# Performance work log

Measured on AMD Instinct MI355X. Metric: run time of the kernel, lower is better.

## Reference

```python
import jax, jax.numpy as jnp
import numpy as np

N = 50176
E = 802816
G = 64
IN_DIM = 128
HID = 128
GLOB = 16
BN_EPS = 1e-5


def transformer_conv(x, src, dst, Wq, bq, Wk, bk, Wv, bv, Ws, bs):
    # PyG TransformerConv, heads=1, concat=True, root_weight=True, beta=False
    q = x @ Wq + bq          # [N, H]
    k = x @ Wk + bk          # [N, H]
    v = x @ Wv + bv          # [N, H]
    scale = 1.0 / jnp.sqrt(jnp.asarray(HID, x.dtype))
    logits = jnp.sum(q[dst] * k[src], axis=-1) * scale          # [E]
    m = jax.ops.segment_max(logits, dst, num_segments=N)        # [N]
    m = jnp.where(jnp.isfinite(m), m, 0.0)
    e = jnp.exp(logits - m[dst])                                # [E]
    s = jax.ops.segment_sum(e, dst, num_segments=N)             # [N]
    alpha = e / (s[dst] + 1e-16)                                # [E]
    agg = jax.ops.segment_sum(alpha[:, None] * v[src], dst, num_segments=N)
    return agg + x @ Ws + bs


def batch_norm(x, gamma, beta):
    mu = jnp.mean(x, axis=0)
    var = jnp.mean((x - mu) ** 2, axis=0)
    return gamma * (x - mu) / jnp.sqrt(var + BN_EPS) + beta


def setup_inputs() -> dict:
    key = jax.random.key(0)
    ks = jax.random.split(key, 32)
    d = {}
    d['x'] = jax.random.normal(ks[0], (N, IN_DIM), dtype=jnp.float32)
    d['edge_index'] = jax.random.randint(ks[1], (2, E), 0, N, dtype=jnp.int32)
    d['ptr'] = (jnp.arange(G + 1, dtype=jnp.int32) * (N // G))
    d['global_features'] = jax.random.normal(ks[2], (G, GLOB), dtype=jnp.float32)
    dims = [(IN_DIM, HID), (HID, HID)]
    ki = 3
    for l, (di, do) in enumerate(dims):
        for nm in ['Wq', 'Wk', 'Wv', 'Ws']:
            d[f'{nm}{l}'] = jax.random.normal(ks[ki], (di, do), dtype=jnp.float32) * 0.05; ki += 1
        for nm in ['bq', 'bk', 'bv', 'bs']:
            d[f'{nm}{l}'] = jnp.zeros((do,), dtype=jnp.float32)
        d[f'g{l}'] = jnp.ones((do,), dtype=jnp.float32)
        d[f'be{l}'] = jnp.zeros((do,), dtype=jnp.float32)
    d['fcW'] = jax.random.normal(ks[ki], (HID + GLOB, HID), dtype=jnp.float32) * 0.05; ki += 1
    d['fcb'] = jnp.zeros((HID,), dtype=jnp.float32)
    d['fc2W'] = jax.random.normal(ks[ki], (HID, 1), dtype=jnp.float32) * 0.05; ki += 1
    d['fc2b'] = jnp.zeros((1,), dtype=jnp.float32)
    return d


def reference(x, edge_index, ptr, global_features,
              Wq0, Wk0, Wv0, Ws0, bq0, bk0, bv0, bs0, g0, be0,
              Wq1, Wk1, Wv1, Ws1, bq1, bk1, bv1, bs1, g1, be1,
              fcW, fcb, fc2W, fc2b):
    src, dst = edge_index[0], edge_index[1]
    h = transformer_conv(x, src, dst, Wq0, bq0, Wk0, bk0, Wv0, bv0, Ws0, bs0)
    h = jax.nn.relu(batch_norm(h, g0, be0))
    h = transformer_conv(h, src, dst, Wq1, bq1, Wk1, bk1, Wv1, bv1, Ws1, bs1)
    h = jax.nn.relu(batch_norm(h, g1, be1))
    # broadcast per-graph global features to nodes using ptr boundaries
    graph_id = jnp.searchsorted(ptr, jnp.arange(N, dtype=ptr.dtype), side='right') - 1
    rep = global_features[graph_id]                              # [N, GLOB]
    h = jnp.concatenate([h, rep], axis=1)
    h = jax.nn.relu(h @ fcW + fcb)
    out = h @ fc2W + fc2b                                        # [N, 1]
    return out[:, 0]
```

## Files before the change

### kernel.cpp

```cpp
#include <hip/hip_runtime.h>
#include <math.h>

#define N_NODES 50176
#define N_EDGES 802816
#define HIDDEN  128
#define NGRAPH  64
#define BN_EPS  1e-5f
#define ATT_SCALE 0.08838834764831845f

typedef __attribute__((ext_vector_type(8))) short bf16x8;
typedef __attribute__((ext_vector_type(4))) float f32x4;

__device__ __forceinline__ float bflo(unsigned u) { return __uint_as_float(u << 16); }
__device__ __forceinline__ float bfhi(unsigned u) { return __uint_as_float(u & 0xffff0000u); }
__device__ __forceinline__ unsigned short f2bf(float f) {
    unsigned u = __float_as_uint(f);
    unsigned r = (u + 0x7fffu + ((u >> 16) & 1u)) >> 16;
    return (unsigned short)r;
}

__global__ void hist_kernel(const int* __restrict__ dst, int* __restrict__ cnt) {
    int e = blockIdx.x * 256 + threadIdx.x;
    if (e < N_EDGES) atomicAdd(&cnt[dst[e]], 1);
}

__global__ void scan1_kernel(const int* __restrict__ cnt, int* __restrict__ row_ptr,
                             int* __restrict__ bsum) {
    __shared__ int sh[256];
    int t = threadIdx.x, b = blockIdx.x;
    int base = b * 1024 + t * 4;
    int v0 = cnt[base], v1 = cnt[base + 1], v2 = cnt[base + 2], v3 = cnt[base + 3];
    int tot = v0 + v1 + v2 + v3;
    sh[t] = tot; __syncthreads();
    for (int off = 1; off < 256; off <<= 1) {
        int x = (t >= off) ? sh[t - off] : 0;
        __syncthreads();
        sh[t] += x;
        __syncthreads();
    }
    int excl = sh[t] - tot;
    row_ptr[base]     = excl;
    row_ptr[base + 1] = excl + v0;
    row_ptr[base + 2] = excl + v0 + v1;
    row_ptr[base + 3] = excl + v0 + v1 + v2;
    if (t == 255) bsum[b] = sh[255];
}

__global__ void scan2_kernel(const int* __restrict__ bsum, int* __restrict__ boff,
                             int* __restrict__ row_ptr) {
    int acc = 0;
    for (int i = 0; i < 49; i++) { boff[i] = acc; acc += bsum[i]; }
    row_ptr[N_NODES] = acc;
}

__global__ void scan3_kernel(int* __restrict__ row_ptr, int* __restrict__ cur,
                             const int* __restrict__ boff) {
    int t = threadIdx.x, b = blockIdx.x;
    int base = b * 1024 + t * 4;
    int off = boff[b];
    #pragma unroll
    for (int j = 0; j < 4; j++) {
        int v = row_ptr[base + j] + off;
        row_ptr[base + j] = v;
        cur[base + j] = v;
    }
}

__global__ void scatter_kernel(const int* __restrict__ src, const int* __restrict__ dst,
                               int* __restrict__ cur, int* __restrict__ edge_src) {
    int e = blockIdx.x * 256 + threadIdx.x;
    if (e < N_EDGES) {
        int d = dst[e];
        int slot = atomicAdd(&cur[d], 1);
        edge_src[slot] = src[e];
    }
}

__global__ void wprep_kernel(const float* __restrict__ Wq, const float* __restrict__ Wk,
                             const float* __restrict__ Wv, const float* __restrict__ Ws,
                             unsigned short* __restrict__ WT) {
    int mb = blockIdx.x;
    const float* W = (mb == 0) ? Wq : (mb == 1) ? Wk : (mb == 2) ? Wv : Ws;
    int t = threadIdx.x;
    int k = t >> 1, ch = t & 1;
    #pragma unroll 8
    for (int cc = 0; cc < 64; cc++) {
        int c = ch * 64 + cc;
        WT[((size_t)mb * 128 + c) * 128 + k] = f2bf(W[k * 128 + c]);
    }
}

__global__ __launch_bounds__(256) void gemm_mfma(
    const float* __restrict__ in,
    const unsigned short* __restrict__ WT,
    const float* __restrict__ bq, const float* __restrict__ bk,
    const float* __restrict__ bv, const float* __restrict__ bs,
    float* __restrict__ qb, unsigned short* __restrict__ kvb,
    float* __restrict__ hb,
    const float* __restrict__ bnA, const float* __restrict__ bnB)
{
    __shared__ unsigned char lds[65536];
    int t = threadIdx.x;
    int n0 = blockIdx.x * 128;
    int m  = blockIdx.y;

    {
        int r = t >> 1, seg = t & 1;
        const float* srcp = in + (size_t)(n0 + r) * 128 + seg * 64;
        unsigned rowbase = r * 256;
        unsigned sw = (r & 7) << 4;
        #pragma unroll
        for (int c = 0; c < 8; c++) {
            float4 f0 = *reinterpret_cast<const float4*>(srcp + c * 8);
            float4 f1 = *reinterpret_cast<const float4*>(srcp + c * 8 + 4);
            if (bnA) {
                int kb = seg * 64 + c * 8;
                float4 a0 = *reinterpret_cast<const float4*>(&bnA[kb]);
                float4 a1 = *reinterpret_cast<const float4*>(&bnA[kb + 4]);
                float4 b0 = *reinterpret_cast<const float4*>(&bnB[kb]);
                float4 b1 = *reinterpret_cast<const float4*>(&bnB[kb + 4]);
                f0.x = fmaxf(f0.x * a0.x + b0.x, 0.f);
                f0.y = fmaxf(f0.y * a0.y + b0.y, 0.f);
                f0.z = fmaxf(f0.z * a0.z + b0.z, 0.f);
                f0.w = fmaxf(f0.w * a0.w + b0.w, 0.f);
                f1.x = fmaxf(f1.x * a1.x + b1.x, 0.f);
                f1.y = fmaxf(f1.y * a1.y + b1.y, 0.f);
                f1.z = fmaxf(f1.z * a1.z + b1.z, 0.f);
                f1.w = fmaxf(f1.w * a1.w + b1.w, 0.f);
            }
            uint4 pk;
            pk.x = (unsigned)f2bf(f0.x) | ((unsigned)f2bf(f0.y) << 16);
            pk.y = (unsigned)f2bf(f0.z) | ((unsigned)f2bf(f0.w) << 16);
            pk.z = (unsigned)f2bf(f1.x) | ((unsigned)f2bf(f1.y) << 16);
            pk.w = (unsigned)f2bf(f1.z) | ((unsigned)f2bf(f1.w) << 16);
            unsigned off = (unsigned)(seg * 128 + c * 16);
            *reinterpret_cast<uint4*>(&lds[rowbase + (off ^ sw)]) = pk;
        }
    }
    {
        int r = t >> 1, seg = t & 1;
        const unsigned short* srcp = WT + ((size_t)m * 128 + r) * 128 + seg * 64;
        unsigned rowbase = 32768u + r * 256;
        unsigned sw = (r & 7) << 4;
        #pragma unroll
        for (int c = 0; c < 8; c++) {
            uint4 pk = *reinterpret_cast<const uint4*>(srcp + c * 8);
            unsigned off = (unsigned)(seg * 128 + c * 16);
            *reinterpret_cast<uint4*>(&lds[rowbase + (off ^ sw)]) = pk;
        }
    }
    __syncthreads();

    int lane = t & 63, w = t >> 6;
    int wr = w >> 1, wc = w & 1;
    int lrow = lane & 15, lk = lane >> 4;
    unsigned sw = (unsigned)((lrow & 7) << 4);

    f32x4 acc[4][4] = {};
    #pragma unroll
    for (int ks = 0; ks < 4; ks++) {
        unsigned o = (unsigned)(ks * 64 + lk * 16);
        bf16x8 af[4], bfr[4];
        #pragma unroll
        for (int i = 0; i < 4; i++) {
            unsigned row = wr * 64 + i * 16 + lrow;
            af[i] = *reinterpret_cast<const bf16x8*>(&lds[row * 256 + (o ^ sw)]);
            unsigned col = wc * 64 + i * 16 + lrow;
            bfr[i] = *reinterpret_cast<const bf16x8*>(&lds[32768u + col * 256 + (o ^ sw)]);
        }
        #pragma unroll
        for (int i = 0; i < 4; i++)
            #pragma unroll
            for (int j = 0; j < 4; j++)
                acc[i][j] = __builtin_amdgcn_mfma_f32_16x16x32_bf16(af[i], bfr[j], acc[i][j], 0, 0, 0);
    }

    const float* bias = (m == 0) ? bq : (m == 1) ? bk : (m == 2) ? bv : bs;
    #pragma unroll
    for (int j = 0; j < 4; j++) {
        int c = wc * 64 + j * 16 + lrow;
        float bi = bias[c];
        #pragma unroll
        for (int i = 0; i < 4; i++) {
            #pragma unroll
            for (int r = 0; r < 4; r++) {
                int row = n0 + wr * 64 + i * 16 + lk * 4 + r;
                float v = acc[i][j][r] + bi;
                if (m == 0) {
                    qb[(size_t)row * 128 + c] = v;
                } else if (m == 3) {
                    hb[(size_t)row * 128 + c] = v;
                } else {
                    kvb[(size_t)row * 256 + (m == 1 ? 0 : 128) + c] = f2bf(v);
                }
            }
        }
    }
}

__global__ __launch_bounds__(256) void agg_kernel(
    const float* __restrict__ qb, const unsigned short* __restrict__ kvb,
    const int* __restrict__ row_ptr, const int* __restrict__ edge_src,
    float* __restrict__ hb)
{
    int wave = threadIdx.x >> 6, lane = threadIdx.x & 63;
    int n = blockIdx.x * 4 + wave;
    int quarter = lane >> 4, ql = lane & 15;

    float4 qa = *reinterpret_cast<const float4*>(&qb[(size_t)n * 128 + ql * 8]);
    float4 qc = *reinterpret_cast<const float4*>(&qb[(size_t)n * 128 + ql * 8 + 4]);
    int s0 = row_ptr[n], s1 = row_ptr[n + 1];

    float acc0 = 0.f, acc1 = 0.f, acc2 = 0.f, acc3 = 0.f;
    float acc4 = 0.f, acc5 = 0.f, acc6 = 0.f, acc7 = 0.f;
    float ssum = 0.f;

    for (int j0 = s0; j0 < s1; j0 += 4) {
        int j = j0 + quarter;
        bool act = (j < s1);
        int s = act ? edge_src[j] : 0;
        const uint4* kv4 = reinterpret_cast<const uint4*>(kvb + (size_t)s * 256);
        uint4 kr = kv4[ql];
        uint4 vr = kv4[16 + ql];

        float part = qa.x * bflo(kr.x) + qa.y * bfhi(kr.x)
                   + qa.z * bflo(kr.y) + qa.w * bfhi(kr.y)
                   + qc.x * bflo(kr.z) + qc.y * bfhi(kr.z)
                   + qc.z * bflo(kr.w) + qc.w * bfhi(kr.w);
        part += __shfl_xor(part, 1, 64);
        part += __shfl_xor(part, 2, 64);
        part += __shfl_xor(part, 4, 64);
        part += __shfl_xor(part, 8, 64);

        float wgt = act ? __expf(part * ATT_SCALE) : 0.f;
        ssum += wgt;
        acc0 += wgt * bflo(vr.x); acc1 += wgt * bfhi(vr.x);
        acc2 += wgt * bflo(vr.y); acc3 += wgt * bfhi(vr.y);
        acc4 += wgt * bflo(vr.z); acc5 += wgt * bfhi(vr.z);
        acc6 += wgt * bflo(vr.w); acc7 += wgt * bfhi(vr.w);
    }

    #define XRED(x) { x += __shfl_xor(x, 16, 64); x += __shfl_xor(x, 32, 64); }
    XRED(acc0) XRED(acc1) XRED(acc2) XRED(acc3)
    XRED(acc4) XRED(acc5) XRED(acc6) XRED(acc7)
    XRED(ssum)
    #undef XRED

    if (quarter == 0) {
        float inv = 1.0f / (ssum + 1e-16f);
        float4 h0 = *reinterpret_cast<float4*>(&hb[(size_t)n * 128 + ql * 8]);
        float4 h1 = *reinterpret_cast<float4*>(&hb[(size_t)n * 128 + ql * 8 + 4]);
        h0.x += acc0 * inv; h0.y += acc1 * inv; h0.z += acc2 * inv; h0.w += acc3 * inv;
        h1.x += acc4 * inv; h1.y += acc5 * inv; h1.z += acc6 * inv; h1.w += acc7 * inv;
        *reinterpret_cast<float4*>(&hb[(size_t)n * 128 + ql * 8]) = h0;
        *reinterpret_cast<float4*>(&hb[(size_t)n * 128 + ql * 8 + 4]) = h1;
    }
}

__global__ __launch_bounds__(256) void bn_stats(const float* __restrict__ h,
                                                float* __restrict__ sums,
                                                float* __restrict__ sqs) {
    int t = threadIdx.x;
    int c = t & 127;
    float s = 0.f, q = 0.f;
    int stride = gridDim.x * 256;
    for (int i = blockIdx.x * 256 + t; i < N_NODES * 128; i += stride) {
        float v = h[i];
        s += v; q += v * v;
    }
    __shared__ float sh[256], shq[256];
    sh[t] = s; shq[t] = q;
    __syncthreads();
    if (t < 128) {
        atomicAdd(&sums[c], sh[t] + sh[t + 128]);
        atomicAdd(&sqs[c],  shq[t] + shq[t + 128]);
    }
}

__global__ void bn_final(const float* __restrict__ sums, const float* __restrict__ sqs,
                         const float* __restrict__ g, const float* __restrict__ be,
                         float* __restrict__ a, float* __restrict__ b) {
    int c = threadIdx.x;
    float mean = sums[c] / (float)N_NODES;
    float var  = sqs[c] / (float)N_NODES - mean * mean;
    float inv  = rsqrtf(var + BN_EPS);
    float av   = g[c] * inv;
    a[c] = av;
    b[c] = be[c] - mean * av;
}

__global__ __launch_bounds__(256) void fc_kernel(
    const float* __restrict__ h2, const float* __restrict__ a1, const float* __restrict__ b1,
    const int* __restrict__ ptr, const float* __restrict__ gf,
    const float* __restrict__ fcW, const float* __restrict__ fcb,
    const float* __restrict__ fc2W, const float* __restrict__ fc2b,
    float* __restrict__ out)
{
    __shared__ float hc[8][144];
    __shared__ float red[8][128];
    int t = threadIdx.x;
    int nb = blockIdx.x * 8;

    {
        int node_l = t >> 5, li = t & 31;
        int n = nb + node_l;
        float4 v = *reinterpret_cast<const float4*>(&h2[(size_t)n * 128 + li * 4]);
        float4 av = *reinterpret_cast<const float4*>(&a1[li * 4]);
        float4 bv = *reinterpret_cast<const float4*>(&b1[li * 4]);
        hc[node_l][li * 4 + 0] = fmaxf(v.x * av.x + bv.x, 0.f);
        hc[node_l][li * 4 + 1] = fmaxf(v.y * av.y + bv.y, 0.f);
        hc[node_l][li * 4 + 2] = fmaxf(v.z * av.z + bv.z, 0.f);
        hc[node_l][li * 4 + 3] = fmaxf(v.w * av.w + bv.w, 0.f);
        if (li < 16) {
            int lo = 0, hi = NGRAPH;
            while (lo < hi) {
                int mid = (lo + hi + 1) >> 1;
                if (ptr[mid] <= n) lo = mid; else hi = mid - 1;
            }
            hc[node_l][128 + li] = gf[lo * 16 + li];
        }
    }
    __syncthreads();

    {
        int half = t >> 7, o = t & 127;
        float fb = fcb[o];
        float acc0 = fb, acc1 = fb, acc2 = fb, acc3 = fb;
        const float* h0 = hc[half * 4 + 0];
        const float* h1 = hc[half * 4 + 1];
        const float* h2c = hc[half * 4 + 2];
        const float* h3 = hc[half * 4 + 3];
        #pragma unroll 16
        for (int i = 0; i < 144; i++) {
            float w = fcW[i * 128 + o];
            acc0 += h0[i] * w;
            acc1 += h1[i] * w;
            acc2 += h2c[i] * w;
            acc3 += h3[i] * w;
        }
        float w2 = fc2W[o];
        red[half * 4 + 0][o] = fmaxf(acc0, 0.f) * w2;
        red[half * 4 + 1][o] = fmaxf(acc1, 0.f) * w2;
        red[half * 4 + 2][o] = fmaxf(acc2, 0.f) * w2;
        red[half * 4 + 3][o] = fmaxf(acc3, 0.f) * w2;
    }
    __syncthreads();

    {
        int node_l = t >> 5, li = t & 31;
        float s = red[node_l][li] + red[node_l][li + 32]
                + red[node_l][li + 64] + red[node_l][li + 96];
        s += __shfl_xor(s, 1, 64);
        s += __shfl_xor(s, 2, 64);
        s += __shfl_xor(s, 4, 64);
        s += __shfl_xor(s, 8, 64);
        s += __shfl_xor(s, 16, 64);
        if (li == 0) out[nb + node_l] = s + fc2b[0];
    }
}

extern "C" void kernel_launch(void* const* d_in, const int* in_sizes, int n_in,
                              void* d_out, int out_size, void* d_ws, size_t ws_size,
                              hipStream_t stream)
{
    const float* x   = (const float*)d_in[0];
    const int*   ei  = (const int*)d_in[1];
    const int*   ptr = (const int*)d_in[2];
    const float* gf  = (const float*)d_in[3];
    const float* Wq0 = (const float*)d_in[4];
    const float* Wk0 = (const float*)d_in[5];
    const float* Wv0 = (const float*)d_in[6];
    const float* Ws0 = (const float*)d_in[7];
    const float* bq0 = (const float*)d_in[8];
    const float* bk0 = (const float*)d_in[9];
    const float* bv0 = (const float*)d_in[10];
    const float* bs0 = (const float*)d_in[11];
    const float* g0  = (const float*)d_in[12];
    const float* be0 = (const float*)d_in[13];
    const float* Wq1 = (const float*)d_in[14];
    const float* Wk1 = (const float*)d_in[15];
    const float* Wv1 = (const float*)d_in[16];
    const float* Ws1 = (const float*)d_in[17];
    const float* bq1 = (const float*)d_in[18];
    const float* bk1 = (const float*)d_in[19];
    const float* bv1 = (const float*)d_in[20];
    const float* bs1 = (const float*)d_in[21];
    const float* g1  = (const float*)d_in[22];
    const float* be1 = (const float*)d_in[23];
    const float* fcW = (const float*)d_in[24];
    const float* fcb = (const float*)d_in[25];
    const float* fc2W= (const float*)d_in[26];
    const float* fc2b= (const float*)d_in[27];
    float* out = (float*)d_out;

    const int* src_p = ei;
    const int* dst_p = ei + N_EDGES;

    char* w = (char*)d_ws;
    const size_t NM = (size_t)N_NODES * 128 * sizeof(float);
    float* qb = (float*)w;                    w += NM;
    unsigned short* kvb = (unsigned short*)w; w += (size_t)N_NODES * 256 * sizeof(unsigned short);
    float* h1 = (float*)w;                    w += NM;
    float* h2 = (float*)w;                    w += NM;
    float* stats = (float*)w;                 w += 1024 * sizeof(float);
    float* sums0 = stats;
    float* sqs0  = stats + 128;
    float* sums1 = stats + 256;
    float* sqs1  = stats + 384;
    float* a0    = stats + 512;
    float* b0    = stats + 640;
    float* a1    = stats + 768;
    float* b1    = stats + 896;
    unsigned short* WT0 = (unsigned short*)w; w += (size_t)512 * 128 * sizeof(unsigned short);
    unsigned short* WT1 = (unsigned short*)w; w += (size_t)512 * 128 * sizeof(unsigned short);
    int* cnt     = (int*)w;                   w += (size_t)N_NODES * sizeof(int);
    int* row_ptr = (int*)w;                   w += (size_t)(N_NODES + 1) * sizeof(int);
    int* cur     = (int*)w;                   w += (size_t)N_NODES * sizeof(int);
    int* edge_src= (int*)w;                   w += (size_t)N_EDGES * sizeof(int);
    int* bsum    = (int*)w;                   w += 64 * sizeof(int);
    int* boff    = (int*)w;                   w += 64 * sizeof(int);

    hipMemsetAsync(cnt, 0, (size_t)N_NODES * sizeof(int), stream);
    hipMemsetAsync(stats, 0, 512 * sizeof(float), stream);

    wprep_kernel<<<4, 256, 0, stream>>>(Wq0, Wk0, Wv0, Ws0, WT0);
    wprep_kernel<<<4, 256, 0, stream>>>(Wq1, Wk1, Wv1, Ws1, WT1);

    hist_kernel<<<3136, 256, 0, stream>>>(dst_p, cnt);
    scan1_kernel<<<49, 256, 0, stream>>>(cnt, row_ptr, bsum);
    scan2_kernel<<<1, 1, 0, stream>>>(bsum, boff, row_ptr);
    scan3_kernel<<<49, 256, 0, stream>>>(row_ptr, cur, boff);
    scatter_kernel<<<3136, 256, 0, stream>>>(src_p, dst_p, cur, edge_src);

    gemm_mfma<<<dim3(392, 4), 256, 0, stream>>>(x, WT0,
        bq0, bk0, bv0, bs0, qb, kvb, h1, nullptr, nullptr);
    agg_kernel<<<12544, 256, 0, stream>>>(qb, kvb, row_ptr, edge_src, h1);
    bn_stats<<<784, 256, 0, stream>>>(h1, sums0, sqs0);
    bn_final<<<1, 128, 0, stream>>>(sums0, sqs0, g0, be0, a0, b0);

    gemm_mfma<<<dim3(392, 4), 256, 0, stream>>>(h1, WT1,
        bq1, bk1, bv1, bs1, qb, kvb, h2, a0, b0);
    agg_kernel<<<12544, 256, 0, stream>>>(qb, kvb, row_ptr, edge_src, h2);
    bn_stats<<<784, 256, 0, stream>>>(h2, sums1, sqs1);
    bn_final<<<1, 128, 0, stream>>>(sums1, sqs1, g1, be1, a1, b1);

    fc_kernel<<<6272, 256, 0, stream>>>(h2, a1, b1, ptr, gf,
        fcW, fcb, fc2W, fc2b, out);
}
```

Baseline: 561.3 us.

## Compute all four projections per block from one shared input tile

The GEMM kernel is restructured so each 512-thread block loads a 64-row input tile once (with fused BN+ReLU and bf16 conversion) and its eight waves compute all four Q/K/V/skip projections, instead of launching a separate block per projection that reloads and reconverts the input. Weight fragments are now read directly from global memory (likely cache-resident) rather than staged in LDS. The K/V bf16 outputs are staged through a swizzled LDS buffer so they can be written to global memory as coalesced 16-byte stores. This cuts input reads and BN work fourfold, at the cost of more global weight traffic per wave and an extra barrier.

```diff
diff --git a/kernel.cpp b/kernel.cpp
--- a/kernel.cpp
+++ b/kernel.cpp
@@ -90,7 +90,7 @@
     }
 }
 
-__global__ __launch_bounds__(256) void gemm_mfma(
+__global__ __launch_bounds__(512, 4) void gemm_mfma(
     const float* __restrict__ in,
     const unsigned short* __restrict__ WT,
     const float* __restrict__ bq, const float* __restrict__ bk,
@@ -99,74 +99,71 @@
     float* __restrict__ hb,
     const float* __restrict__ bnA, const float* __restrict__ bnB)
 {
-    __shared__ unsigned char lds[65536];
+    __shared__ unsigned char ldsA[16384];
+    __shared__ unsigned char ldsKV[32768];
     int t = threadIdx.x;
-    int n0 = blockIdx.x * 128;
-    int m  = blockIdx.y;
+    int n0 = blockIdx.x * 64;
 
     {
-        int r = t >> 1, seg = t & 1;
-        const float* srcp = in + (size_t)(n0 + r) * 128 + seg * 64;
-        unsigned rowbase = r * 256;
-        unsigned sw = (r & 7) << 4;
-        #pragma unroll
-        for (int c = 0; c < 8; c++) {
-            float4 f0 = *reinterpret_cast<const float4*>(srcp + c * 8);
-            float4 f1 = *reinterpret_cast<const float4*>(srcp + c * 8 + 4);
-            if (bnA) {
-                int kb = seg * 64 + c * 8;
-                float4 a0 = *reinterpret_cast<const float4*>(&bnA[kb]);
-                float4 a1 = *reinterpret_cast<const float4*>(&bnA[kb + 4]);
-                float4 b0 = *reinterpret_cast<const float4*>(&bnB[kb]);
-                float4 b1 = *reinterpret_cast<const float4*>(&bnB[kb + 4]);
-                f0.x = fmaxf(f0.x * a0.x + b0.x, 0.f);
-                f0.y = fmaxf(f0.y * a0.y + b0.y, 0.f);
-                f0.z = fmaxf(f0.z * a0.z + b0.z, 0.f);
-                f0.w = fmaxf(f0.w * a0.w + b0.w, 0.f);
-                f1.x = fmaxf(f1.x * a1.x + b1.x, 0.f);
-                f1.y = fmaxf(f1.y * a1.y + b1.y, 0.f);
-                f1.z = fmaxf(f1.z * a1.z + b1.z, 0.f);
-                f1.w = fmaxf(f1.w * a1.w + b1.w, 0.f);
-            }
-            uint4 pk;
-            pk.x = (unsigned)f2bf(f0.x) | ((unsigned)f2bf(f0.y) << 16);
-            pk.y = (unsigned)f2bf(f0.z) | ((unsigned)f2bf(f0.w) << 16);
-            pk.z = (unsigned)f2bf(f1.x) | ((unsigned)f2bf(f1.y) << 16);
-            pk.w = (unsigned)f2bf(f1.z) | ((unsigned)f2bf(f1.w) << 16);
-            unsigned off = (unsigned)(seg * 128 + c * 16);
-            *reinterpret_cast<uint4*>(&lds[rowbase + (off ^ sw)]) = pk;
-        }
-    }
-    {
-        int r = t >> 1, seg = t & 1;
-        const unsigned short* srcp = WT + ((size_t)m * 128 + r) * 128 + seg * 64;
-        unsigned rowbase = 32768u + r * 256;
-        unsigned sw = (r & 7) << 4;
-        #pragma unroll
-        for (int c = 0; c < 8; c++) {
-            uint4 pk = *reinterpret_cast<const uint4*>(srcp + c * 8);
-            unsigned off = (unsigned)(seg * 128 + c * 16);
-            *reinterpret_cast<uint4*>(&lds[rowbase + (off ^ sw)]) = pk;
-        }
+        int r = t >> 3, seg = t & 7;
+        const float* srcp = in + (size_t)(n0 + r) * 128 + seg * 16;
+        float4 f0 = *reinterpret_cast<const float4*>(srcp);
+        float4 f1 = *reinterpret_cast<const float4*>(srcp + 4);
+        float4 f2 = *reinterpret_cast<const float4*>(srcp + 8);
+        float4 f3 = *reinterpret_cast<const float4*>(srcp + 12);
+        if (bnA) {
+            int kb = seg * 16;
+            float4 a0 = *reinterpret_cast<const float4*>(&bnA[kb]);
+            float4 a1 = *reinterpret_cast<const float4*>(&bnA[kb + 4]);
+            float4 a2 = *reinterpret_cast<const float4*>(&bnA[kb + 8]);
+            float4 a3 = *reinterpret_cast<const float4*>(&bnA[kb + 12]);
+            float4 b0 = *reinterpret_cast<const float4*>(&bnB[kb]);
+            float4 b1 = *reinterpret_cast<const float4*>(&bnB[kb + 4]);
+            float4 b2 = *reinterpret_cast<const float4*>(&bnB[kb + 8]);
+            float4 b3 = *reinterpret_cast<const float4*>(&bnB[kb + 12]);
+            f0.x = fmaxf(f0.x * a0.x + b0.x, 0.f); f0.y = fmaxf(f0.y * a0.y + b0.y, 0.f);
+            f0.z = fmaxf(f0.z * a0.z + b0.z, 0.f); f0.w = fmaxf(f0.w * a0.w + b0.w, 0.f);
+            f1.x = fmaxf(f1.x * a1.x + b1.x, 0.f); f1.y = fmaxf(f1.y * a1.y + b1.y, 0.f);
+            f1.z = fmaxf(f1.z * a1.z + b1.z, 0.f); f1.w = fmaxf(f1.w * a1.w + b1.w, 0.f);
+            f2.x = fmaxf(f2.x * a2.x + b2.x, 0.f); f2.y = fmaxf(f2.y * a2.y + b2.y, 0.f);
+            f2.z = fmaxf(f2.z * a2.z + b2.z, 0.f); f2.w = fmaxf(f2.w * a2.w + b2.w, 0.f);
+            f3.x = fmaxf(f3.x * a3.x + b3.x, 0.f); f3.y = fmaxf(f3.y * a3.y + b3.y, 0.f);
+            f3.z = fmaxf(f3.z * a3.z + b3.z, 0.f); f3.w = fmaxf(f3.w * a3.w + b3.w, 0.f);
+        }
+        uint4 p0, p1;
+        p0.x = (unsigned)f2bf(f0.x) | ((unsigned)f2bf(f0.y) << 16);
+        p0.y = (unsigned)f2bf(f0.z) | ((unsigned)f2bf(f0.w) << 16);
+        p0.z = (unsigned)f2bf(f1.x) | ((unsigned)f2bf(f1.y) << 16);
+        p0.w = (unsigned)f2bf(f1.z) | ((unsigned)f2bf(f1.w) << 16);
+        p1.x = (unsigned)f2bf(f2.x) | ((unsigned)f2bf(f2.y) << 16);
+        p1.y = (unsigned)f2bf(f2.z) | ((unsigned)f2bf(f2.w) << 16);
+        p1.z = (unsigned)f2bf(f3.x) | ((unsigned)f2bf(f3.y) << 16);
+        p1.w = (unsigned)f2bf(f3.z) | ((unsigned)f2bf(f3.w) << 16);
+        unsigned sw = (unsigned)((r & 7) << 4);
+        *reinterpret_cast<uint4*>(&ldsA[r * 256 + (((unsigned)(seg * 32)) ^ sw)]) = p0;
+        *reinterpret_cast<uint4*>(&ldsA[r * 256 + (((unsigned)(seg * 32 + 16)) ^ sw)]) = p1;
     }
     __syncthreads();
 
     int lane = t & 63, w = t >> 6;
-    int wr = w >> 1, wc = w & 1;
+    int m = w >> 1, half = w & 1;
     int lrow = lane & 15, lk = lane >> 4;
-    unsigned sw = (unsigned)((lrow & 7) << 4);
 
     f32x4 acc[4][4] = {};
     #pragma unroll
     for (int ks = 0; ks < 4; ks++) {
-        unsigned o = (unsigned)(ks * 64 + lk * 16);
-        bf16x8 af[4], bfr[4];
+        bf16x8 bfr[4], af[4];
+        #pragma unroll
+        for (int j = 0; j < 4; j++) {
+            int col = half * 64 + j * 16 + lrow;
+            bfr[j] = *reinterpret_cast<const bf16x8*>(
+                &WT[((size_t)m * 128 + col) * 128 + ks * 32 + lk * 8]);
+        }
         #pragma unroll
         for (int i = 0; i < 4; i++) {
-            unsigned row = wr * 64 + i * 16 + lrow;
-            af[i] = *reinterpret_cast<const bf16x8*>(&lds[row * 256 + (o ^ sw)]);
-            unsigned col = wc * 64 + i * 16 + lrow;
-            bfr[i] = *reinterpret_cast<const bf16x8*>(&lds[32768u + col * 256 + (o ^ sw)]);
+            unsigned row = (unsigned)(i * 16 + lrow);
+            af[i] = *reinterpret_cast<const bf16x8*>(
+                &ldsA[row * 256 + (((unsigned)(ks * 64 + lk * 16)) ^ ((row & 7) << 4))]);
         }
         #pragma unroll
         for (int i = 0; i < 4; i++)
@@ -176,24 +173,48 @@
     }
 
     const float* bias = (m == 0) ? bq : (m == 1) ? bk : (m == 2) ? bv : bs;
-    #pragma unroll
-    for (int j = 0; j < 4; j++) {
-        int c = wc * 64 + j * 16 + lrow;
-        float bi = bias[c];
-        #pragma unroll
-        for (int i = 0; i < 4; i++) {
+    if (m == 0 || m == 3) {
+        float* ob = (m == 0) ? qb : hb;
+        #pragma unroll
+        for (int j = 0; j < 4; j++) {
+            int c = half * 64 + j * 16 + lrow;
+            float bi = bias[c];
             #pragma unroll
-            for (int r = 0; r < 4; r++) {
-                int row = n0 + wr * 64 + i * 16 + lk * 4 + r;
-                float v = acc[i][j][r] + bi;
-                if (m == 0) {
-                    qb[(size_t)row * 128 + c] = v;
-                } else if (m == 3) {
-                    hb[(size_t)row * 128 + c] = v;
-                } else {
-                    kvb[(size_t)row * 256 + (m == 1 ? 0 : 128) + c] = f2bf(v);
+            for (int i = 0; i < 4; i++)
+                #pragma unroll
+                for (int r4 = 0; r4 < 4; r4++) {
+                    int row = n0 + i * 16 + lk * 4 + r4;
+                    ob[(size_t)row * 128 + c] = acc[i][j][r4] + bi;
                 }
-            }
+        }
+    } else {
+        unsigned vOff = (m == 1) ? 0u : 256u;
+        #pragma unroll
+        for (int j = 0; j < 4; j++) {
+            int c = half * 64 + j * 16 + lrow;
+            float bi = bias[c];
+            unsigned bir = vOff + (unsigned)c * 2;
+            #pragma unroll
+            for (int i = 0; i < 4; i++)
+                #pragma unroll
+                for (int r4 = 0; r4 < 4; r4++) {
+                    unsigned row = (unsigned)(i * 16 + lk * 4 + r4);
+                    unsigned sw = ((row >> 2) & 3) << 5;
+                    *reinterpret_cast<unsigned short*>(&ldsKV[row * 512 + (bir ^ sw)]) =
+                        f2bf(acc[i][j][r4] + bi);
+                }
+        }
+    }
+    __syncthreads();
+    {
+        int r = t >> 3, seg = t & 7;
+        unsigned sw = (((unsigned)r >> 2) & 3) << 5;
+        char* dst = (char*)(kvb + (size_t)(n0 + r) * 256) + seg * 64;
+        #pragma unroll
+        for (int u = 0; u < 4; u++) {
+            uint4 v = *reinterpret_cast<const uint4*>(
+                &ldsKV[r * 512 + (((unsigned)(seg * 64 + u * 16)) ^ sw)]);
+            *reinterpret_cast<uint4*>(dst + u * 16) = v;
         }
     }
 }
@@ -432,13 +453,13 @@
     scan3_kernel<<<49, 256, 0, stream>>>(row_ptr, cur, boff);
     scatter_kernel<<<3136, 256, 0, stream>>>(src_p, dst_p, cur, edge_src);
 
-    gemm_mfma<<<dim3(392, 4), 256, 0, stream>>>(x, WT0,
+    gemm_mfma<<<784, 512, 0, stream>>>(x, WT0,
         bq0, bk0, bv0, bs0, qb, kvb, h1, nullptr, nullptr);
     agg_kernel<<<12544, 256, 0, stream>>>(qb, kvb, row_ptr, edge_src, h1);
     bn_stats<<<784, 256, 0, stream>>>(h1, sums0, sqs0);
     bn_final<<<1, 128, 0, stream>>>(sums0, sqs0, g0, be0, a0, b0);
 
-    gemm_mfma<<<dim3(392, 4), 256, 0, stream>>>(h1, WT1,
+    gemm_mfma<<<784, 512, 0, stream>>>(h1, WT1,
         bq1, bk1, bv1, bs1, qb, kvb, h2, a0, b0);
     agg_kernel<<<12544, 256, 0, stream>>>(qb, kvb, row_ptr, edge_src, h2);
     bn_stats<<<784, 256, 0, stream>>>(h2, sums1, sqs1);
```

Result: faster. 519.4 us (-7.5%).
